# Optimization experiments

Measured on AMD Instinct MI355X. Metric: run time of the kernel, lower is better.

The kernel has to match this reference:

```python
import jax, jax.numpy as jnp
import numpy as np

B, H, N, C, E, D, L_OUT, LAYERS = 16, 64, 512, 3, 128, 32, 12, 2


def setup_inputs() -> dict:
    key = jax.random.key(0)
    ks = jax.random.split(key, 16)
    nrm = lambda k, s, sc=1.0: jax.random.normal(k, s, jnp.float32) * sc
    adj = jax.random.uniform(ks[0], (N, N), jnp.float32)
    adj = adj / adj.sum(axis=-1, keepdims=True)  # row-normalized prior adjacency
    return {
        "x_input": nrm(ks[1], (B, H, N, C)),
        "adj": adj,
        "Wf": nrm(ks[2], (3, E, 3 * C), 0.1),
        "Uf": nrm(ks[3], (3, E, E), 0.05),
        "bf": jnp.zeros((3, E), jnp.float32),
        "E1f": nrm(ks[4], (N, D)),
        "E2f": nrm(ks[5], (N, D)),
        "Wb": nrm(ks[6], (3, E, 3 * C), 0.1),
        "Ub": nrm(ks[7], (3, E, E), 0.05),
        "bb": jnp.zeros((3, E), jnp.float32),
        "E1b": nrm(ks[8], (N, D)),
        "E2b": nrm(ks[9], (N, D)),
        "dec_w": nrm(ks[10], (L_OUT, LAYERS, 2 * E), 0.05),  # Conv2d(layer_num->out_len, k=(1,2E)) squeezed
        "dec_b": jnp.zeros((L_OUT,), jnp.float32),
        "out_w": nrm(ks[11], (L_OUT, L_OUT), 0.1),  # 1x1 Conv2d squeezed
        "out_b": jnp.zeros((L_OUT,), jnp.float32),
    }


def _cell_step(c, xt, adj, A_dyn, W, U, b):
    # Graph-coupled GRU cell (IBNCell): xt [B,C,N], c [B,E,N].
    msg = jnp.concatenate(
        [xt,
         jnp.einsum('bcn,nm->bcm', xt, adj),      # prior-graph message passing
         jnp.einsum('bcn,nm->bcm', xt, A_dyn)],   # learned dynamic-graph message passing
        axis=1)  # [B, 3C, N]
    gx = jnp.einsum('goc,bcn->gbon', W, msg)  # 3 stacked gate projections
    r = jax.nn.sigmoid(gx[0] + jnp.einsum('oe,ben->bon', U[0], c) + b[0][:, None])
    u = jax.nn.sigmoid(gx[1] + jnp.einsum('oe,ben->bon', U[1], c) + b[1][:, None])
    g = jnp.tanh(gx[2] + jnp.einsum('oe,ben->bon', U[2], r * c) + b[2][:, None])
    return u * c + (1.0 - u) * g


def _forward(x_input, adj, Wf, Uf, bf, E1f, E2f, Wb, Ub, bb, E1b, E2b, dec_w, dec_b, out_w, out_b):
    # torch: x_input.transpose(-3,-1).transpose(-2,-1) -> [B,C,H,N]; scan layout [H,B,C,N]
    xs = jnp.transpose(x_input, (1, 0, 3, 2))
    A_f = jax.nn.softmax(jax.nn.relu(E1f @ E2f.T), axis=-1)  # dynamic adjacency, fwd cell
    A_b = jax.nn.softmax(jax.nn.relu(E1b @ E2b.T), axis=-1)  # dynamic adjacency, back cell
    c0 = jnp.zeros((xs.shape[1], Wf.shape[1], xs.shape[3]), xs.dtype)  # [B,E,N]

    def step_f(c, xt):
        cn = _cell_step(c, xt, adj, A_f, Wf, Uf, bf)
        return cn, None

    # Output only depends on the last timestep of the bidirectional concat:
    # forward branch -> final state after H steps; backward branch (after flip)
    # at t=H-1 -> its FIRST step (input x[H-1]). Dead per-step outputs elided.
    h_fwd, _ = jax.lax.scan(step_f, c0, xs)
    h_back0 = _cell_step(c0, xs[-1], adj, A_b, Wb, Ub, bb)
    last_ht = jnp.concatenate([h_fwd, h_back0], axis=1)  # [B, 2E, N]

    lt = jnp.transpose(last_ht, (0, 2, 1))  # [B, N, 2E]
    # layer loop z>0 is a no-op on current_layer_output -> final_result repeats last_ht
    final = jnp.broadcast_to(lt[:, None], (lt.shape[0], LAYERS, lt.shape[1], lt.shape[2]))
    h = jnp.einsum('blne,ole->bon', final, dec_w) + dec_b[:, None]  # decoder conv (1,2E)
    return jnp.einsum('oi,bin->bon', out_w, h) + out_b[:, None]  # 1x1 output conv -> [B,L_OUT,N]


def reference(x_input, adj, Wf, Uf, bf, E1f, E2f, Wb, Ub, bb, E1b, E2b, dec_w, dec_b, out_w, out_b):
    return _forward(x_input, adj, Wf, Uf, bf, E1f, E2f, Wb, Ub, bb, E1b, E2b, dec_w, dec_b, out_w, out_b)
```

## Files before the change

kernel.cpp:

```cpp
#include <hip/hip_runtime.h>


typedef _Float16 half8_t __attribute__((ext_vector_type(8)));
typedef float float4_t __attribute__((ext_vector_type(4)));

__device__ __forceinline__ float sigmoidf_(float x) {
  return __builtin_amdgcn_rcpf(1.f + __expf(-x));
}
__device__ __forceinline__ float tanhf_(float x) {
  return fmaf(-2.f, __builtin_amdgcn_rcpf(__expf(2.f * x) + 1.f), 1.f);
}

__global__ __launch_bounds__(256) void prep_kernel(
    const float* __restrict__ E1f, const float* __restrict__ E2f,
    const float* __restrict__ E1b, const float* __restrict__ E2b,
    const float* __restrict__ adj, const float* __restrict__ Wf,
    const float* __restrict__ Uf, const float* __restrict__ bf,
    const float* __restrict__ Wb, const float* __restrict__ bb,
    _Float16* __restrict__ adjT, _Float16* __restrict__ AfT,
    _Float16* __restrict__ AbT, _Float16* __restrict__ ufrag,
    _Float16* __restrict__ wbfrag) {
  int bid = blockIdx.x;
  int tid = threadIdx.x;
  if (bid >= 1272) {
    int r2 = bid - 1272;
    int gi = 1 + (r2 & 1);
    int rt = (r2 >> 1) & 1;
    int og = r2 >> 2;
    for (int e = tid; e < 512; e += 256) {
      int lane = e >> 3, j = e & 7;
      int o = og * 32 + rt * 16 + (lane & 15);
      int q = (lane >> 4) * 8 + j;
      float v = (q < 9) ? Wb[gi * 1152 + o * 9 + q]
                        : (q == 9 ? bb[gi * 128 + o] : 0.f);
      wbfrag[r2 * 512 + e] = (_Float16)v;
    }
    return;
  }
  if (bid >= 1152) {
    int r = bid - 1152;
    int kb = r % 5;
    int gi = (r / 5) % 3;
    int rt = (r / 15) % 2;
    int og = r / 30;
    for (int e = tid; e < 512; e += 256) {
      int lane = e >> 3, j = e & 7;
      int o = og * 32 + rt * 16 + (lane & 15);
      int q4 = lane >> 4;
      float v;
      if (kb < 4) {
        v = Uf[gi * 16384 + o * 128 + kb * 32 + q4 * 8 + j];
      } else {
        int q = q4 * 8 + j;
        v = (q < 9) ? Wf[gi * 1152 + o * 9 + q]
                    : (q == 9 ? bf[gi * 128 + o] : 0.f);
      }
      ufrag[r * 512 + e] = (_Float16)v;
    }
    return;
  }
  if (bid >= 1024) {
    int base = (bid - 1024) * 4;
    for (int r = 0; r < 4; ++r) {
      int row = base + r;
      float v0 = adj[row * 512 + tid];
      float v1 = adj[row * 512 + tid + 256];
      adjT[(size_t)tid * 512 + row] = (_Float16)v0;
      adjT[(size_t)(tid + 256) * 512 + row] = (_Float16)v1;
    }
    return;
  }
  int which = bid >> 9;
  int row = bid & 511;
  const float* E1 = which ? E1b : E1f;
  const float* E2 = which ? E2b : E2f;
  _Float16* A = which ? AbT : AfT;
  __shared__ float e1s[32];
  __shared__ float red[256];
  if (tid < 32) e1s[tid] = E1[row * 32 + tid];
  __syncthreads();
  float s[2];
#pragma unroll
  for (int h = 0; h < 2; ++h) {
    int m = tid + h * 256;
    const float4* e2 = (const float4*)(E2 + m * 32);
    float acc = 0.f;
#pragma unroll
    for (int d4 = 0; d4 < 8; ++d4) {
      float4 v = e2[d4];
      acc = fmaf(v.x, e1s[d4 * 4 + 0], acc);
      acc = fmaf(v.y, e1s[d4 * 4 + 1], acc);
      acc = fmaf(v.z, e1s[d4 * 4 + 2], acc);
      acc = fmaf(v.w, e1s[d4 * 4 + 3], acc);
    }
    s[h] = fmaxf(acc, 0.f);
  }
  red[tid] = fmaxf(s[0], s[1]);
  __syncthreads();
  for (int off = 128; off > 0; off >>= 1) {
    if (tid < off) red[tid] = fmaxf(red[tid], red[tid + off]);
    __syncthreads();
  }
  float mx = red[0];
  __syncthreads();
  float e0 = __expf(s[0] - mx), e1v = __expf(s[1] - mx);
  red[tid] = e0 + e1v;
  __syncthreads();
  for (int off = 128; off > 0; off >>= 1) {
    if (tid < off) red[tid] += red[tid + off];
    __syncthreads();
  }
  float inv = __builtin_amdgcn_rcpf(red[0]);
  A[(size_t)tid * 512 + row] = (_Float16)(e0 * inv);
  A[(size_t)(tid + 256) * 512 + row] = (_Float16)(e1v * inv);
}

__global__ __launch_bounds__(256, 2) void msg_kernel(
    const float* __restrict__ x, const _Float16* __restrict__ adjT,
    const _Float16* __restrict__ AfT, const _Float16* __restrict__ AbT,
    _Float16* __restrict__ msg16, _Float16* __restrict__ msgb16) {
  __shared__ __align__(16) _Float16 Alds[48 * 512];
  __shared__ __align__(16) _Float16 Sst[16 * 64 * 16];
  int tid = threadIdx.x;
  int t = blockIdx.x >> 3;
  int n0g = (blockIdx.x & 7) * 64;
  int lane = tid & 63, og = tid >> 6;
  int l15 = lane & 15, q4 = lane >> 4, q0 = q4 * 8;
  bool is63 = (t == 63);

  {
    int b = tid >> 4, li = tid & 15;
    const float4* xb = (const float4*)(x + (size_t)(b * 64 + t) * 1536);
#pragma unroll
    for (int k = 0; k < 24; ++k) {
      float4 v = xb[k * 16 + li];
      int j0 = (k * 16 + li) * 4;
#pragma unroll
      for (int e = 0; e < 4; ++e) {
        int j = j0 + e;
        int n = (j * 21846) >> 16;
        int c = j - n * 3;
        int m = b * 3 + c;
        float val = (e == 0) ? v.x : (e == 1) ? v.y : (e == 2) ? v.z : v.w;
        Alds[m * 512 + ((((n >> 3) ^ (m & 7)) << 3) | (n & 7))] = (_Float16)val;
      }
    }
  }
  __syncthreads();

  const float4_t zero4 = {0.f, 0.f, 0.f, 0.f};
  float4_t acc[3][2], accb[3];
#pragma unroll
  for (int mt = 0; mt < 3; ++mt) { acc[mt][0] = zero4; acc[mt][1] = zero4; accb[mt] = zero4; }

  int n = n0g + og * 16 + l15;
  for (int kb = 0; kb < 16; ++kb) {
    half8_t afr[3];
#pragma unroll
    for (int mt = 0; mt < 3; ++mt) {
      int m = mt * 16 + l15;
      afr[mt] = *(const half8_t*)&Alds[m * 512 + ((((kb * 4 + q4) ^ (m & 7)) << 3))];
    }
    half8_t b0 = *(const half8_t*)&adjT[(size_t)n * 512 + kb * 32 + q0];
    half8_t b1 = *(const half8_t*)&AfT[(size_t)n * 512 + kb * 32 + q0];
#pragma unroll
    for (int mt = 0; mt < 3; ++mt) {
      acc[mt][0] = __builtin_amdgcn_mfma_f32_16x16x32_f16(afr[mt], b0, acc[mt][0], 0, 0, 0);
      acc[mt][1] = __builtin_amdgcn_mfma_f32_16x16x32_f16(afr[mt], b1, acc[mt][1], 0, 0, 0);
    }
    if (is63) {
      half8_t b2 = *(const half8_t*)&AbT[(size_t)n * 512 + kb * 32 + q0];
#pragma unroll
      for (int mt = 0; mt < 3; ++mt)
        accb[mt] = __builtin_amdgcn_mfma_f32_16x16x32_f16(afr[mt], b2, accb[mt], 0, 0, 0);
    }
  }

  for (int i = tid; i < 1024; i += 256) {
    int tb = i >> 6, nl = i & 63;
    int nn = n0g + nl;
    _Float16* row = &Sst[(tb * 64 + nl) * 16];
#pragma unroll
    for (int c = 0; c < 3; ++c) {
      int m = tb * 3 + c;
      row[c] = Alds[m * 512 + ((((nn >> 3) ^ (m & 7)) << 3) | (nn & 7))];
    }
    row[9] = (_Float16)1.f;
#pragma unroll
    for (int kz = 10; kz < 16; ++kz) row[kz] = (_Float16)0.f;
  }
#pragma unroll
  for (int mt = 0; mt < 3; ++mt)
#pragma unroll
    for (int r = 0; r < 4; ++r) {
      int m = mt * 16 + q4 * 4 + r;
      int tb = (m * 21846) >> 16;
      int c = m - tb * 3;
      _Float16* row = &Sst[(tb * 64 + og * 16 + l15) * 16];
      row[3 + c] = (_Float16)acc[mt][0][r];
      row[6 + c] = (_Float16)acc[mt][1][r];
    }
  __syncthreads();
  for (int i = tid; i < 1024; i += 256) {
    int tb = i >> 6, nl = i & 63;
    uint4* dst = (uint4*)&msg16[((size_t)(t * 16 + tb) * 512 + n0g + nl) * 16];
    const uint4* s = (const uint4*)&Sst[(tb * 64 + nl) * 16];
    dst[0] = s[0];
    dst[1] = s[1];
  }
  if (is63) {
    __syncthreads();
#pragma unroll
    for (int mt = 0; mt < 3; ++mt)
#pragma unroll
      for (int r = 0; r < 4; ++r) {
        int m = mt * 16 + q4 * 4 + r;
        int tb = (m * 21846) >> 16;
        int c = m - tb * 3;
        Sst[(tb * 64 + og * 16 + l15) * 16 + 6 + c] = (_Float16)accb[mt][r];
      }
    __syncthreads();
    for (int i = tid; i < 1024; i += 256) {
      int tb = i >> 6, nl = i & 63;
      uint4* dst = (uint4*)&msgb16[((size_t)tb * 512 + n0g + nl) * 16];
      const uint4* s = (const uint4*)&Sst[(tb * 64 + nl) * 16];
      dst[0] = s[0];
      dst[1] = s[1];
    }
  }
}

__global__ __launch_bounds__(256, 2) __attribute__((amdgpu_waves_per_eu(2, 2)))
void rec_kernel(
    const _Float16* __restrict__ msg16, const _Float16* __restrict__ msgb16,
    const _Float16* __restrict__ ufrag, const _Float16* __restrict__ wbfrag,
    const float* __restrict__ dec_w, const float* __restrict__ dec_b,
    const float* __restrict__ out_w, const float* __restrict__ out_b,
    float* __restrict__ out) {
  __shared__ __align__(16) _Float16 Bmsg[64 * 16 * 16];
  __shared__ __align__(16) _Float16 Cbuf[4 * 64 * 8];
  __shared__ __align__(16) _Float16 Gbuf[4 * 64 * 8];
  __shared__ float hf_lds[128 * 16];
  __shared__ float hb_lds[128 * 16];
  __shared__ float hdec_lds[12 * 16];
  int tid = threadIdx.x, bid = blockIdx.x;
  int b = bid >> 5;
  int n0 = (bid & 31) * 16;
  int lane = tid & 63, og = tid >> 6;
  int l15 = lane & 15, q4 = lane >> 4;

  half8_t afrag[3][2][5];
#pragma unroll
  for (int gi = 0; gi < 3; ++gi)
#pragma unroll
    for (int rt = 0; rt < 2; ++rt)
#pragma unroll
      for (int kb = 0; kb < 5; ++kb)
        afrag[gi][rt][kb] = *(const half8_t*)
            &ufrag[(size_t)((((og * 2 + rt) * 3 + gi) * 5 + kb) * 512) + lane * 8];

  {
    const uint4* src = (const uint4*)msg16;
    uint4* dst = (uint4*)Bmsg;
    for (int f = tid; f < 2048; f += 256) {
      int t = f >> 5, off = f & 31;
      int nn = off >> 1, h = off & 1;
      dst[t * 32 + nn * 2 + (h ^ (nn & 1))] =
          src[((size_t)(t * 16 + b) * 512 + n0) * 2 + off];
    }
  }
  {
    uint4 z; z.x = z.y = z.z = z.w = 0;
    ((uint4*)Cbuf)[tid] = z;
  }
  float cr[2][4];
#pragma unroll
  for (int rt = 0; rt < 2; ++rt)
#pragma unroll
    for (int r = 0; r < 4; ++r) cr[rt][r] = 0.f;
  __syncthreads();

  const float4_t zero4 = {0.f, 0.f, 0.f, 0.f};
  union H4U { _Float16 h[4]; unsigned long long u; };
  int bm_off = l15 * 16 + (((q4 & 1) ^ (l15 & 1)) << 3);

  for (int t = 0; t < 64; ++t) {
    half8_t bmsg = *(const half8_t*)&Bmsg[t * 256 + bm_off];
    half8_t cf[4];
#pragma unroll
    for (int kb = 0; kb < 4; ++kb)
      cf[kb] = *(const half8_t*)&Cbuf[(kb * 64 + lane) * 8];

    float4_t accr[2], accu[2];
    accr[0] = accr[1] = accu[0] = accu[1] = zero4;
#pragma unroll
    for (int kb = 0; kb < 4; ++kb)
#pragma unroll
      for (int rt = 0; rt < 2; ++rt) {
        accr[rt] = __builtin_amdgcn_mfma_f32_16x16x32_f16(afrag[0][rt][kb], cf[kb], accr[rt], 0, 0, 0);
        accu[rt] = __builtin_amdgcn_mfma_f32_16x16x32_f16(afrag[1][rt][kb], cf[kb], accu[rt], 0, 0, 0);
      }
#pragma unroll
    for (int rt = 0; rt < 2; ++rt) {
      accr[rt] = __builtin_amdgcn_mfma_f32_16x16x32_f16(afrag[0][rt][4], bmsg, accr[rt], 0, 0, 0);
      accu[rt] = __builtin_amdgcn_mfma_f32_16x16x32_f16(afrag[1][rt][4], bmsg, accu[rt], 0, 0, 0);
    }
#pragma unroll
    for (int rt = 0; rt < 2; ++rt) {
      H4U v;
#pragma unroll
      for (int r = 0; r < 4; ++r)
        v.h[r] = (_Float16)(sigmoidf_(accr[rt][r]) * cr[rt][r]);
      int lane_t = (rt * 2 + (q4 >> 1)) * 16 + l15;
      *(unsigned long long*)&Gbuf[(og * 64 + lane_t) * 8 + (q4 & 1) * 4] = v.u;
    }
    __syncthreads();

    half8_t gf[4];
#pragma unroll
    for (int kb = 0; kb < 4; ++kb)
      gf[kb] = *(const half8_t*)&Gbuf[(kb * 64 + lane) * 8];
    float4_t accg[2];
#pragma unroll
    for (int rt = 0; rt < 2; ++rt) {
      float4_t a = zero4;
#pragma unroll
      for (int kb = 0; kb < 4; ++kb)
        a = __builtin_amdgcn_mfma_f32_16x16x32_f16(afrag[2][rt][kb], gf[kb], a, 0, 0, 0);
      a = __builtin_amdgcn_mfma_f32_16x16x32_f16(afrag[2][rt][4], bmsg, a, 0, 0, 0);
      accg[rt] = a;
    }
#pragma unroll
    for (int rt = 0; rt < 2; ++rt) {
      H4U v;
#pragma unroll
      for (int r = 0; r < 4; ++r) {
        float uu = sigmoidf_(accu[rt][r]);
        float gg = tanhf_(accg[rt][r]);
        float cn = fmaf(uu, cr[rt][r] - gg, gg);
        cr[rt][r] = cn;
        v.h[r] = (_Float16)cn;
      }
      int lane_t = (rt * 2 + (q4 >> 1)) * 16 + l15;
      *(unsigned long long*)&Cbuf[(og * 64 + lane_t) * 8 + (q4 & 1) * 4] = v.u;
    }
    __syncthreads();
  }

  {
    half8_t bbk = *(const half8_t*)
        &msgb16[((size_t)b * 512 + n0 + l15) * 16 + (q4 & 1) * 8];
#pragma unroll
    for (int rt = 0; rt < 2; ++rt) {
      half8_t au_f = *(const half8_t*)&wbfrag[(size_t)(((og * 2 + rt) * 2 + 0) * 512) + lane * 8];
      half8_t ag_f = *(const half8_t*)&wbfrag[(size_t)(((og * 2 + rt) * 2 + 1) * 512) + lane * 8];
      float4_t au = __builtin_amdgcn_mfma_f32_16x16x32_f16(au_f, bbk, zero4, 0, 0, 0);
      float4_t ag = __builtin_amdgcn_mfma_f32_16x16x32_f16(ag_f, bbk, zero4, 0, 0, 0);
#pragma unroll
      for (int r = 0; r < 4; ++r) {
        int row = og * 32 + rt * 16 + q4 * 4 + r;
        float uu = sigmoidf_(au[r]);
        float gg = tanhf_(ag[r]);
        hb_lds[row * 16 + l15] = (1.f - uu) * gg;
        hf_lds[row * 16 + l15] = cr[rt][r];
      }
    }
  }
  __syncthreads();

  if (tid < 192) {
    int i = tid >> 4, cc = tid & 15;
    const float* dwa = dec_w + (size_t)i * 512;
    const float* dwb = dwa + 256;
    float hd = dec_b[i];
    for (int e = 0; e < 128; ++e) {
      hd = fmaf(dwa[e] + dwb[e], hf_lds[e * 16 + cc], hd);
      hd = fmaf(dwa[128 + e] + dwb[128 + e], hb_lds[e * 16 + cc], hd);
    }
    hdec_lds[i * 16 + cc] = hd;
  }
  __syncthreads();
  if (tid < 192) {
    int o = tid >> 4, cc = tid & 15;
    float v = out_b[o];
#pragma unroll
    for (int i = 0; i < 12; ++i) v = fmaf(out_w[o * 12 + i], hdec_lds[i * 16 + cc], v);
    out[((size_t)(b * 12 + o)) * 512 + n0 + cc] = v;
  }
}

extern "C" void kernel_launch(void* const* d_in, const int* in_sizes, int n_in,
                              void* d_out, int out_size, void* d_ws, size_t ws_size,
                              hipStream_t stream) {
  (void)in_sizes; (void)n_in; (void)out_size; (void)ws_size;
  const float* x     = (const float*)d_in[0];
  const float* adj   = (const float*)d_in[1];
  const float* Wf    = (const float*)d_in[2];
  const float* Uf    = (const float*)d_in[3];
  const float* bf    = (const float*)d_in[4];
  const float* E1f   = (const float*)d_in[5];
  const float* E2f   = (const float*)d_in[6];
  const float* Wb    = (const float*)d_in[7];
  const float* bb    = (const float*)d_in[9];
  const float* E1b   = (const float*)d_in[10];
  const float* E2b   = (const float*)d_in[11];
  const float* dec_w = (const float*)d_in[12];
  const float* dec_b = (const float*)d_in[13];
  const float* out_w = (const float*)d_in[14];
  const float* out_b = (const float*)d_in[15];

  _Float16* h      = (_Float16*)d_ws;
  _Float16* adjT   = h;
  _Float16* AfT    = h + 262144;
  _Float16* AbT    = h + 524288;
  _Float16* msg16  = h + 786432;
  _Float16* msgb16 = h + 9175040;
  _Float16* ufrag  = h + 9306112;
  _Float16* wbfrag = h + 9367552;

  prep_kernel<<<1288, 256, 0, stream>>>(E1f, E2f, E1b, E2b, adj, Wf, Uf, bf,
                                        Wb, bb, adjT, AfT, AbT, ufrag, wbfrag);
  msg_kernel<<<512, 256, 0, stream>>>(x, adjT, AfT, AbT, msg16, msgb16);
  rec_kernel<<<512, 256, 0, stream>>>(msg16, msgb16, ufrag, wbfrag,
                                      dec_w, dec_b, out_w, out_b, (float*)d_out);
}
```

Measured before the change: 214.7 us.

## Restructure message and recurrence kernels: transposed fp16 x, packed msg, 512-thread recurrence

A new prep stage writes x to global memory as transposed fp16. The message kernel then reads its A operand from global memory instead of staging it in LDS, splits the adjacency matrices across waves, and runs twice as many smaller blocks. The message record shrinks from 16 to 12 halves, which cuts msg write and read traffic. The recurrence kernel now uses 512 threads per block, each wave owning 16 output rows instead of 32, and prefetches the next timestep's msg from global memory instead of preloading it into LDS, trading shorter per-wave serial MFMA chains for more waves per barrier.

Result: slower. 220.0 us (+2.5%).

```diff
diff --git a/kernel.cpp b/kernel.cpp
--- a/kernel.cpp
+++ b/kernel.cpp
@@ -3,6 +3,8 @@
 
 typedef _Float16 half8_t __attribute__((ext_vector_type(8)));
 typedef float float4_t __attribute__((ext_vector_type(4)));
+
+#define PIN(x) asm volatile("" : "+v"(x))
 
 __device__ __forceinline__ float sigmoidf_(float x) {
   return __builtin_amdgcn_rcpf(1.f + __expf(-x));
@@ -14,22 +16,37 @@
 __global__ __launch_bounds__(256) void prep_kernel(
     const float* __restrict__ E1f, const float* __restrict__ E2f,
     const float* __restrict__ E1b, const float* __restrict__ E2b,
-    const float* __restrict__ adj, const float* __restrict__ Wf,
-    const float* __restrict__ Uf, const float* __restrict__ bf,
-    const float* __restrict__ Wb, const float* __restrict__ bb,
-    _Float16* __restrict__ adjT, _Float16* __restrict__ AfT,
-    _Float16* __restrict__ AbT, _Float16* __restrict__ ufrag,
+    const float* __restrict__ adj, const float* __restrict__ x,
+    const float* __restrict__ Wf, const float* __restrict__ Uf,
+    const float* __restrict__ bf, const float* __restrict__ Wb,
+    const float* __restrict__ bb, _Float16* __restrict__ adjT,
+    _Float16* __restrict__ AfT, _Float16* __restrict__ AbT,
+    _Float16* __restrict__ xT16, _Float16* __restrict__ ufrag,
     _Float16* __restrict__ wbfrag) {
   int bid = blockIdx.x;
   int tid = threadIdx.x;
+  if (bid >= 1288) {
+    int bid2 = bid - 1288;
+    int b = bid2 >> 6, t = bid2 & 63;
+    const float2* xp = (const float2*)(x + (size_t)(b * 64 + t) * 1536);
+    float2 f0 = xp[tid * 3], f1 = xp[tid * 3 + 1], f2 = xp[tid * 3 + 2];
+    _Float16* dst = xT16 + (size_t)(b * 64 + t) * 1536;
+    int n0_ = tid * 2;
+    dst[n0_] = (_Float16)f0.x;
+    dst[512 + n0_] = (_Float16)f0.y;
+    dst[1024 + n0_] = (_Float16)f1.x;
+    dst[n0_ + 1] = (_Float16)f1.y;
+    dst[512 + n0_ + 1] = (_Float16)f2.x;
+    dst[1024 + n0_ + 1] = (_Float16)f2.y;
+    return;
+  }
   if (bid >= 1272) {
     int r2 = bid - 1272;
     int gi = 1 + (r2 & 1);
-    int rt = (r2 >> 1) & 1;
-    int og = r2 >> 2;
+    int og = r2 >> 1;
     for (int e = tid; e < 512; e += 256) {
       int lane = e >> 3, j = e & 7;
-      int o = og * 32 + rt * 16 + (lane & 15);
+      int o = og * 16 + (lane & 15);
       int q = (lane >> 4) * 8 + j;
       float v = (q < 9) ? Wb[gi * 1152 + o * 9 + q]
                         : (q == 9 ? bb[gi * 128 + o] : 0.f);
@@ -41,11 +58,10 @@
     int r = bid - 1152;
     int kb = r % 5;
     int gi = (r / 5) % 3;
-    int rt = (r / 15) % 2;
-    int og = r / 30;
+    int og = r / 15;
     for (int e = tid; e < 512; e += 256) {
       int lane = e >> 3, j = e & 7;
-      int o = og * 32 + rt * 16 + (lane & 15);
+      int o = og * 16 + (lane & 15);
       int q4 = lane >> 4;
       float v;
       if (kb < 4) {
@@ -115,79 +131,55 @@
   A[(size_t)(tid + 256) * 512 + row] = (_Float16)(e1v * inv);
 }
 
-__global__ __launch_bounds__(256, 2) void msg_kernel(
-    const float* __restrict__ x, const _Float16* __restrict__ adjT,
+__global__ __launch_bounds__(256, 4) void msg_kernel(
+    const _Float16* __restrict__ xT16, const _Float16* __restrict__ adjT,
     const _Float16* __restrict__ AfT, const _Float16* __restrict__ AbT,
     _Float16* __restrict__ msg16, _Float16* __restrict__ msgb16) {
-  __shared__ __align__(16) _Float16 Alds[48 * 512];
-  __shared__ __align__(16) _Float16 Sst[16 * 64 * 16];
+  __shared__ __align__(8) _Float16 Sst[512 * 12];
   int tid = threadIdx.x;
-  int t = blockIdx.x >> 3;
-  int n0g = (blockIdx.x & 7) * 64;
+  int t = blockIdx.x >> 4;
+  int n0g = (blockIdx.x & 15) * 32;
   int lane = tid & 63, og = tid >> 6;
   int l15 = lane & 15, q4 = lane >> 4, q0 = q4 * 8;
+  int nt = og & 1, mat = og >> 1;
   bool is63 = (t == 63);
-
-  {
-    int b = tid >> 4, li = tid & 15;
-    const float4* xb = (const float4*)(x + (size_t)(b * 64 + t) * 1536);
-#pragma unroll
-    for (int k = 0; k < 24; ++k) {
-      float4 v = xb[k * 16 + li];
-      int j0 = (k * 16 + li) * 4;
-#pragma unroll
-      for (int e = 0; e < 4; ++e) {
-        int j = j0 + e;
-        int n = (j * 21846) >> 16;
-        int c = j - n * 3;
-        int m = b * 3 + c;
-        float val = (e == 0) ? v.x : (e == 1) ? v.y : (e == 2) ? v.z : v.w;
-        Alds[m * 512 + ((((n >> 3) ^ (m & 7)) << 3) | (n & 7))] = (_Float16)val;
-      }
-    }
-  }
-  __syncthreads();
+  bool doAb = is63 && (mat == 0);
+
+  const _Float16* Bmat = mat ? AfT : adjT;
+  int n = n0g + nt * 16 + l15;
 
   const float4_t zero4 = {0.f, 0.f, 0.f, 0.f};
-  float4_t acc[3][2], accb[3];
-#pragma unroll
-  for (int mt = 0; mt < 3; ++mt) { acc[mt][0] = zero4; acc[mt][1] = zero4; accb[mt] = zero4; }
-
-  int n = n0g + og * 16 + l15;
+  float4_t acc[3], accb[3];
+#pragma unroll
+  for (int mt = 0; mt < 3; ++mt) { acc[mt] = zero4; accb[mt] = zero4; }
+
   for (int kb = 0; kb < 16; ++kb) {
-    half8_t afr[3];
+    half8_t b0 = *(const half8_t*)&Bmat[(size_t)n * 512 + kb * 32 + q0];
+    half8_t b2;
+    if (doAb) b2 = *(const half8_t*)&AbT[(size_t)n * 512 + kb * 32 + q0];
 #pragma unroll
     for (int mt = 0; mt < 3; ++mt) {
       int m = mt * 16 + l15;
-      afr[mt] = *(const half8_t*)&Alds[m * 512 + ((((kb * 4 + q4) ^ (m & 7)) << 3))];
-    }
-    half8_t b0 = *(const half8_t*)&adjT[(size_t)n * 512 + kb * 32 + q0];
-    half8_t b1 = *(const half8_t*)&AfT[(size_t)n * 512 + kb * 32 + q0];
-#pragma unroll
-    for (int mt = 0; mt < 3; ++mt) {
-      acc[mt][0] = __builtin_amdgcn_mfma_f32_16x16x32_f16(afr[mt], b0, acc[mt][0], 0, 0, 0);
-      acc[mt][1] = __builtin_amdgcn_mfma_f32_16x16x32_f16(afr[mt], b1, acc[mt][1], 0, 0, 0);
-    }
-    if (is63) {
-      half8_t b2 = *(const half8_t*)&AbT[(size_t)n * 512 + kb * 32 + q0];
-#pragma unroll
-      for (int mt = 0; mt < 3; ++mt)
-        accb[mt] = __builtin_amdgcn_mfma_f32_16x16x32_f16(afr[mt], b2, accb[mt], 0, 0, 0);
-    }
-  }
-
-  for (int i = tid; i < 1024; i += 256) {
-    int tb = i >> 6, nl = i & 63;
+      int bm = (m * 21846) >> 16;
+      int cm = m - bm * 3;
+      half8_t a = *(const half8_t*)
+          &xT16[((size_t)(bm * 64 + t) * 3 + cm) * 512 + kb * 32 + q0];
+      acc[mt] = __builtin_amdgcn_mfma_f32_16x16x32_f16(a, b0, acc[mt], 0, 0, 0);
+      if (doAb)
+        accb[mt] = __builtin_amdgcn_mfma_f32_16x16x32_f16(a, b2, accb[mt], 0, 0, 0);
+    }
+  }
+
+  for (int i = tid; i < 512; i += 256) {
+    int tb = i >> 5, nl = i & 31;
     int nn = n0g + nl;
-    _Float16* row = &Sst[(tb * 64 + nl) * 16];
-#pragma unroll
-    for (int c = 0; c < 3; ++c) {
-      int m = tb * 3 + c;
-      row[c] = Alds[m * 512 + ((((nn >> 3) ^ (m & 7)) << 3) | (nn & 7))];
-    }
+    _Float16* row = &Sst[i * 12];
+#pragma unroll
+    for (int c = 0; c < 3; ++c)
+      row[c] = xT16[((size_t)(tb * 64 + t) * 3 + c) * 512 + nn];
     row[9] = (_Float16)1.f;
-#pragma unroll
-    for (int kz = 10; kz < 16; ++kz) row[kz] = (_Float16)0.f;
+    row[10] = (_Float16)0.f;
+    row[11] = (_Float16)0.f;
   }
 #pragma unroll
   for (int mt = 0; mt < 3; ++mt)
@@ -196,48 +188,45 @@
       int m = mt * 16 + q4 * 4 + r;
       int tb = (m * 21846) >> 16;
       int c = m - tb * 3;
-      _Float16* row = &Sst[(tb * 64 + og * 16 + l15) * 16];
-      row[3 + c] = (_Float16)acc[mt][0][r];
-      row[6 + c] = (_Float16)acc[mt][1][r];
-    }
-  __syncthreads();
-  for (int i = tid; i < 1024; i += 256) {
-    int tb = i >> 6, nl = i & 63;
-    uint4* dst = (uint4*)&msg16[((size_t)(t * 16 + tb) * 512 + n0g + nl) * 16];
-    const uint4* s = (const uint4*)&Sst[(tb * 64 + nl) * 16];
-    dst[0] = s[0];
-    dst[1] = s[1];
+      Sst[((size_t)tb * 32 + nt * 16 + l15) * 12 + 3 + mat * 3 + c] =
+          (_Float16)acc[mt][r];
+    }
+  __syncthreads();
+  for (int i = tid; i < 512; i += 256) {
+    int tb = i >> 5, nl = i & 31;
+    const uint2* s = (const uint2*)&Sst[i * 12];
+    uint2* dst = (uint2*)&msg16[((size_t)(t * 16 + tb) * 512 + n0g + nl) * 12];
+    dst[0] = s[0]; dst[1] = s[1]; dst[2] = s[2];
   }
   if (is63) {
     __syncthreads();
-#pragma unroll
-    for (int mt = 0; mt < 3; ++mt)
-#pragma unroll
-      for (int r = 0; r < 4; ++r) {
-        int m = mt * 16 + q4 * 4 + r;
-        int tb = (m * 21846) >> 16;
-        int c = m - tb * 3;
-        Sst[(tb * 64 + og * 16 + l15) * 16 + 6 + c] = (_Float16)accb[mt][r];
-      }
-    __syncthreads();
-    for (int i = tid; i < 1024; i += 256) {
-      int tb = i >> 6, nl = i & 63;
-      uint4* dst = (uint4*)&msgb16[((size_t)tb * 512 + n0g + nl) * 16];
-      const uint4* s = (const uint4*)&Sst[(tb * 64 + nl) * 16];
-      dst[0] = s[0];
-      dst[1] = s[1];
-    }
-  }
-}
-
-__global__ __launch_bounds__(256, 2) __attribute__((amdgpu_waves_per_eu(2, 2)))
-void rec_kernel(
+    if (mat == 0) {
+#pragma unroll
+      for (int mt = 0; mt < 3; ++mt)
+#pragma unroll
+        for (int r = 0; r < 4; ++r) {
+          int m = mt * 16 + q4 * 4 + r;
+          int tb = (m * 21846) >> 16;
+          int c = m - tb * 3;
+          Sst[((size_t)tb * 32 + nt * 16 + l15) * 12 + 6 + c] = (_Float16)accb[mt][r];
+        }
+    }
+    __syncthreads();
+    for (int i = tid; i < 512; i += 256) {
+      int tb = i >> 5, nl = i & 31;
+      const uint2* s = (const uint2*)&Sst[i * 12];
+      uint2* dst = (uint2*)&msgb16[((size_t)tb * 512 + n0g + nl) * 12];
+      dst[0] = s[0]; dst[1] = s[1]; dst[2] = s[2];
+    }
+  }
+}
+
+__global__ __launch_bounds__(512, 4) void rec_kernel(
     const _Float16* __restrict__ msg16, const _Float16* __restrict__ msgb16,
     const _Float16* __restrict__ ufrag, const _Float16* __restrict__ wbfrag,
     const float* __restrict__ dec_w, const float* __restrict__ dec_b,
     const float* __restrict__ out_w, const float* __restrict__ out_b,
     float* __restrict__ out) {
-  __shared__ __align__(16) _Float16 Bmsg[64 * 16 * 16];
   __shared__ __align__(16) _Float16 Cbuf[4 * 64 * 8];
   __shared__ __align__(16) _Float16 Gbuf[4 * 64 * 8];
   __shared__ float hf_lds[128 * 16];
@@ -249,70 +238,72 @@
   int lane = tid & 63, og = tid >> 6;
   int l15 = lane & 15, q4 = lane >> 4;
 
-  half8_t afrag[3][2][5];
+  half8_t afrag[3][5];
 #pragma unroll
   for (int gi = 0; gi < 3; ++gi)
 #pragma unroll
-    for (int rt = 0; rt < 2; ++rt)
-#pragma unroll
-      for (int kb = 0; kb < 5; ++kb)
-        afrag[gi][rt][kb] = *(const half8_t*)
-            &ufrag[(size_t)((((og * 2 + rt) * 3 + gi) * 5 + kb) * 512) + lane * 8];
-
-  {
-    const uint4* src = (const uint4*)msg16;
-    uint4* dst = (uint4*)Bmsg;
-    for (int f = tid; f < 2048; f += 256) {
-      int t = f >> 5, off = f & 31;
-      int nn = off >> 1, h = off & 1;
-      dst[t * 32 + nn * 2 + (h ^ (nn & 1))] =
-          src[((size_t)(t * 16 + b) * 512 + n0) * 2 + off];
-    }
-  }
-  {
+    for (int kb = 0; kb < 5; ++kb) {
+      afrag[gi][kb] = *(const half8_t*)
+          &ufrag[(size_t)(((og * 3 + gi) * 5 + kb) * 512) + lane * 8];
+      PIN(afrag[gi][kb]);
+    }
+
+  if (tid < 256) {
     uint4 z; z.x = z.y = z.z = z.w = 0;
     ((uint4*)Cbuf)[tid] = z;
   }
-  float cr[2][4];
-#pragma unroll
-  for (int rt = 0; rt < 2; ++rt)
-#pragma unroll
-    for (int r = 0; r < 4; ++r) cr[rt][r] = 0.f;
+  float cr[4] = {0.f, 0.f, 0.f, 0.f};
   __syncthreads();
 
   const float4_t zero4 = {0.f, 0.f, 0.f, 0.f};
   union H4U { _Float16 h[4]; unsigned long long u; };
-  int bm_off = l15 * 16 + (((q4 & 1) ^ (l15 & 1)) << 3);
+  union U16 { uint4 u4; half8_t h8; };
+  unsigned odd = q4 & 1;
+  const char* mrow = (const char*)msg16 + ((size_t)(b * 512 + n0 + l15)) * 24;
+  const size_t tstride = (size_t)16 * 512 * 24;
+
+  U16 bu;
+  {
+    uint4 lo = *(const uint4*)mrow;
+    uint2 hi = *(const uint2*)(mrow + 16);
+    bu.u4.x = odd ? hi.x : lo.x;
+    bu.u4.y = odd ? hi.y : lo.y;
+    bu.u4.z = odd ? 0u : lo.z;
+    bu.u4.w = odd ? 0u : lo.w;
+  }
+  half8_t bm_cur = bu.h8;
+
+  int kb_w = og >> 1;
+  int lane_w = ((og & 1) * 2 + (q4 >> 1)) * 16 + l15;
+  int j0 = (q4 & 1) * 4;
 
   for (int t = 0; t < 64; ++t) {
-    half8_t bmsg = *(const half8_t*)&Bmsg[t * 256 + bm_off];
+    int tn = (t < 63) ? t + 1 : 63;
+    const char* p = mrow + (size_t)tn * tstride;
+    uint4 lo = *(const uint4*)p;
+    uint2 hi = *(const uint2*)(p + 16);
+
     half8_t cf[4];
 #pragma unroll
     for (int kb = 0; kb < 4; ++kb)
       cf[kb] = *(const half8_t*)&Cbuf[(kb * 64 + lane) * 8];
 
-    float4_t accr[2], accu[2];
-    accr[0] = accr[1] = accu[0] = accu[1] = zero4;
-#pragma unroll
-    for (int kb = 0; kb < 4; ++kb)
-#pragma unroll
-      for (int rt = 0; rt < 2; ++rt) {
-        accr[rt] = __builtin_amdgcn_mfma_f32_16x16x32_f16(afrag[0][rt][kb], cf[kb], accr[rt], 0, 0, 0);
-        accu[rt] = __builtin_amdgcn_mfma_f32_16x16x32_f16(afrag[1][rt][kb], cf[kb], accu[rt], 0, 0, 0);
-      }
-#pragma unroll
-    for (int rt = 0; rt < 2; ++rt) {
-      accr[rt] = __builtin_amdgcn_mfma_f32_16x16x32_f16(afrag[0][rt][4], bmsg, accr[rt], 0, 0, 0);
-      accu[rt] = __builtin_amdgcn_mfma_f32_16x16x32_f16(afrag[1][rt][4], bmsg, accu[rt], 0, 0, 0);
-    }
-#pragma unroll
-    for (int rt = 0; rt < 2; ++rt) {
+    float4_t accr = zero4, accu = zero4;
+#pragma unroll
+    for (int kb = 0; kb < 4; ++kb) {
+      accr = __builtin_amdgcn_mfma_f32_16x16x32_f16(afrag[0][kb], cf[kb], accr, 0, 0, 0);
+      accu = __builtin_amdgcn_mfma_f32_16x16x32_f16(afrag[1][kb], cf[kb], accu, 0, 0, 0);
+    }
+    accr = __builtin_amdgcn_mfma_f32_16x16x32_f16(afrag[0][4], bm_cur, accr, 0, 0, 0);
+    accu = __builtin_amdgcn_mfma_f32_16x16x32_f16(afrag[1][4], bm_cur, accu, 0, 0, 0);
+    float4_t accg = __builtin_amdgcn_mfma_f32_16x16x32_f16(afrag[2][4], bm_cur, zero4, 0, 0, 0);
+
+    {
       H4U v;
 #pragma unroll
       for (int r = 0; r < 4; ++r)
-        v.h[r] = (_Float16)(sigmoidf_(accr[rt][r]) * cr[rt][r]);
-      int lane_t = (rt * 2 + (q4 >> 1)) * 16 + l15;
-      *(unsigned long long*)&Gbuf[(og * 64 + lane_t) * 8 + (q4 & 1) * 4] = v.u;
+        v.h[r] = (_Float16)(sigmoidf_(accr[r]) * cr[r]);
+      *(unsigned long long*)&Gbuf[(kb_w * 64 + lane_w) * 8 + j0] = v.u;
     }
     __syncthreads();
 
@@ -320,50 +311,51 @@
 #pragma unroll
     for (int kb = 0; kb < 4; ++kb)
       gf[kb] = *(const half8_t*)&Gbuf[(kb * 64 + lane) * 8];
-    float4_t accg[2];
-#pragma unroll
-    for (int rt = 0; rt < 2; ++rt) {
-      float4_t a = zero4;
-#pragma unroll
-      for (int kb = 0; kb < 4; ++kb)
-        a = __builtin_amdgcn_mfma_f32_16x16x32_f16(afrag[2][rt][kb], gf[kb], a, 0, 0, 0);
-      a = __builtin_amdgcn_mfma_f32_16x16x32_f16(afrag[2][rt][4], bmsg, a, 0, 0, 0);
-      accg[rt] = a;
-    }
-#pragma unroll
-    for (int rt = 0; rt < 2; ++rt) {
+#pragma unroll
+    for (int kb = 0; kb < 4; ++kb)
+      accg = __builtin_amdgcn_mfma_f32_16x16x32_f16(afrag[2][kb], gf[kb], accg, 0, 0, 0);
+
+    {
       H4U v;
 #pragma unroll
       for (int r = 0; r < 4; ++r) {
-        float uu = sigmoidf_(accu[rt][r]);
-        float gg = tanhf_(accg[rt][r]);
-        float cn = fmaf(uu, cr[rt][r] - gg, gg);
-        cr[rt][r] = cn;
+        float uu = sigmoidf_(accu[r]);
+        float gg = tanhf_(accg[r]);
+        float cn = fmaf(uu, cr[r] - gg, gg);
+        cr[r] = cn;
         v.h[r] = (_Float16)cn;
       }
-      int lane_t = (rt * 2 + (q4 >> 1)) * 16 + l15;
-      *(unsigned long long*)&Cbuf[(og * 64 + lane_t) * 8 + (q4 & 1) * 4] = v.u;
-    }
-    __syncthreads();
+      *(unsigned long long*)&Cbuf[(kb_w * 64 + lane_w) * 8 + j0] = v.u;
+    }
+    __syncthreads();
+
+    bu.u4.x = odd ? hi.x : lo.x;
+    bu.u4.y = odd ? hi.y : lo.y;
+    bu.u4.z = odd ? 0u : lo.z;
+    bu.u4.w = odd ? 0u : lo.w;
+    bm_cur = bu.h8;
   }
 
   {
-    half8_t bbk = *(const half8_t*)
-        &msgb16[((size_t)b * 512 + n0 + l15) * 16 + (q4 & 1) * 8];
-#pragma unroll
-    for (int rt = 0; rt < 2; ++rt) {
-      half8_t au_f = *(const half8_t*)&wbfrag[(size_t)(((og * 2 + rt) * 2 + 0) * 512) + lane * 8];
-      half8_t ag_f = *(const half8_t*)&wbfrag[(size_t)(((og * 2 + rt) * 2 + 1) * 512) + lane * 8];
-      float4_t au = __builtin_amdgcn_mfma_f32_16x16x32_f16(au_f, bbk, zero4, 0, 0, 0);
-      float4_t ag = __builtin_amdgcn_mfma_f32_16x16x32_f16(ag_f, bbk, zero4, 0, 0, 0);
-#pragma unroll
-      for (int r = 0; r < 4; ++r) {
-        int row = og * 32 + rt * 16 + q4 * 4 + r;
-        float uu = sigmoidf_(au[r]);
-        float gg = tanhf_(ag[r]);
-        hb_lds[row * 16 + l15] = (1.f - uu) * gg;
-        hf_lds[row * 16 + l15] = cr[rt][r];
-      }
+    const char* p = (const char*)msgb16 + ((size_t)(b * 512 + n0 + l15)) * 24;
+    uint4 lo = *(const uint4*)p;
+    uint2 hi = *(const uint2*)(p + 16);
+    U16 bb2;
+    bb2.u4.x = odd ? hi.x : lo.x;
+    bb2.u4.y = odd ? hi.y : lo.y;
+    bb2.u4.z = odd ? 0u : lo.z;
+    bb2.u4.w = odd ? 0u : lo.w;
+    half8_t au_f = *(const half8_t*)&wbfrag[(size_t)((og * 2 + 0) * 512) + lane * 8];
+    half8_t ag_f = *(const half8_t*)&wbfrag[(size_t)((og * 2 + 1) * 512) + lane * 8];
+    float4_t au = __builtin_amdgcn_mfma_f32_16x16x32_f16(au_f, bb2.h8, zero4, 0, 0, 0);
+    float4_t ag = __builtin_amdgcn_mfma_f32_16x16x32_f16(ag_f, bb2.h8, zero4, 0, 0, 0);
+#pragma unroll
+    for (int r = 0; r < 4; ++r) {
+      int row = og * 16 + q4 * 4 + r;
+      float uu = sigmoidf_(au[r]);
+      float gg = tanhf_(ag[r]);
+      hb_lds[row * 16 + l15] = (1.f - uu) * gg;
+      hf_lds[row * 16 + l15] = cr[r];
     }
   }
   __syncthreads();
@@ -413,14 +405,15 @@
   _Float16* adjT   = h;
   _Float16* AfT    = h + 262144;
   _Float16* AbT    = h + 524288;
-  _Float16* msg16  = h + 786432;
-  _Float16* msgb16 = h + 9175040;
-  _Float16* ufrag  = h + 9306112;
-  _Float16* wbfrag = h + 9367552;
-
-  prep_kernel<<<1288, 256, 0, stream>>>(E1f, E2f, E1b, E2b, adj, Wf, Uf, bf,
-                                        Wb, bb, adjT, AfT, AbT, ufrag, wbfrag);
-  msg_kernel<<<512, 256, 0, stream>>>(x, adjT, AfT, AbT, msg16, msgb16);
-  rec_kernel<<<512, 256, 0, stream>>>(msg16, msgb16, ufrag, wbfrag,
+  _Float16* xT16   = h + 786432;
+  _Float16* ufrag  = h + 2359296;
+  _Float16* wbfrag = h + 2420736;
+  _Float16* msg16  = h + 2428928;
+  _Float16* msgb16 = h + 8720384;
+
+  prep_kernel<<<2312, 256, 0, stream>>>(E1f, E2f, E1b, E2b, adj, x, Wf, Uf, bf,
+                                        Wb, bb, adjT, AfT, AbT, xT16, ufrag, wbfrag);
+  msg_kernel<<<1024, 256, 0, stream>>>(xT16, adjT, AfT, AbT, msg16, msgb16);
+  rec_kernel<<<512, 512, 0, stream>>>(msg16, msgb16, ufrag, wbfrag,
                                       dec_w, dec_b, out_w, out_b, (float*)d_out);
 }
```

## Split recurrent GRU rows across 8 waves, stream messages from global in fragment layout

Applied to the files above, without the earlier changes.

The recurrent kernel now runs 512 threads per block, so each wave owns one 16-row output tile instead of two. That halves the serial MFMA chain and activation work per wave on every timestep. The message tensor is written by msg_kernel directly in MFMA fragment order and prefetched one step ahead from global memory, which removes the LDS staging buffer and its fill loop. Log2(e) scaling is folded into the gate weights so sigmoid and tanh use raw exp2 and rcp, and fp16 packing uses cvt_pkrtz. The cost is higher register pressure and more waves taking part in each per-step block barrier.

New measurement: 203.0 us. 5.4% less time.

```diff
diff --git a/kernel.cpp b/kernel.cpp
--- a/kernel.cpp
+++ b/kernel.cpp
@@ -2,14 +2,13 @@
 
 
 typedef _Float16 half8_t __attribute__((ext_vector_type(8)));
+typedef __fp16 fp16x2_t __attribute__((ext_vector_type(2)));
 typedef float float4_t __attribute__((ext_vector_type(4)));
 
-__device__ __forceinline__ float sigmoidf_(float x) {
-  return __builtin_amdgcn_rcpf(1.f + __expf(-x));
-}
-__device__ __forceinline__ float tanhf_(float x) {
-  return fmaf(-2.f, __builtin_amdgcn_rcpf(__expf(2.f * x) + 1.f), 1.f);
-}
+#define PIN(x) asm volatile("" : "+v"(x))
+
+__device__ __forceinline__ float exp2_(float x) { return __builtin_amdgcn_exp2f(x); }
+__device__ __forceinline__ float rcp_(float x) { return __builtin_amdgcn_rcpf(x); }
 
 __global__ __launch_bounds__(256) void prep_kernel(
     const float* __restrict__ E1f, const float* __restrict__ E2f,
@@ -25,15 +24,15 @@
   if (bid >= 1272) {
     int r2 = bid - 1272;
     int gi = 1 + (r2 & 1);
-    int rt = (r2 >> 1) & 1;
-    int og = r2 >> 2;
+    int og = r2 >> 1;
+    float scl = (gi == 2) ? 2.8853902f : -1.4426950f;
     for (int e = tid; e < 512; e += 256) {
       int lane = e >> 3, j = e & 7;
-      int o = og * 32 + rt * 16 + (lane & 15);
+      int o = og * 16 + (lane & 15);
       int q = (lane >> 4) * 8 + j;
       float v = (q < 9) ? Wb[gi * 1152 + o * 9 + q]
                         : (q == 9 ? bb[gi * 128 + o] : 0.f);
-      wbfrag[r2 * 512 + e] = (_Float16)v;
+      wbfrag[r2 * 512 + e] = (_Float16)(v * scl);
     }
     return;
   }
@@ -41,11 +40,11 @@
     int r = bid - 1152;
     int kb = r % 5;
     int gi = (r / 5) % 3;
-    int rt = (r / 15) % 2;
-    int og = r / 30;
+    int og = r / 15;
+    float scl = (gi == 2) ? 2.8853902f : -1.4426950f;
     for (int e = tid; e < 512; e += 256) {
       int lane = e >> 3, j = e & 7;
-      int o = og * 32 + rt * 16 + (lane & 15);
+      int o = og * 16 + (lane & 15);
       int q4 = lane >> 4;
       float v;
       if (kb < 4) {
@@ -55,7 +54,7 @@
         v = (q < 9) ? Wf[gi * 1152 + o * 9 + q]
                     : (q == 9 ? bf[gi * 128 + o] : 0.f);
       }
-      ufrag[r * 512 + e] = (_Float16)v;
+      ufrag[r * 512 + e] = (_Float16)(v * scl);
     }
     return;
   }
@@ -110,7 +109,7 @@
     if (tid < off) red[tid] += red[tid + off];
     __syncthreads();
   }
-  float inv = __builtin_amdgcn_rcpf(red[0]);
+  float inv = rcp_(red[0]);
   A[(size_t)tid * 512 + row] = (_Float16)(e0 * inv);
   A[(size_t)(tid + 256) * 512 + row] = (_Float16)(e1v * inv);
 }
@@ -118,12 +117,13 @@
 __global__ __launch_bounds__(256, 2) void msg_kernel(
     const float* __restrict__ x, const _Float16* __restrict__ adjT,
     const _Float16* __restrict__ AfT, const _Float16* __restrict__ AbT,
-    _Float16* __restrict__ msg16, _Float16* __restrict__ msgb16) {
+    _Float16* __restrict__ msgF, _Float16* __restrict__ msgbF) {
   __shared__ __align__(16) _Float16 Alds[48 * 512];
-  __shared__ __align__(16) _Float16 Sst[16 * 64 * 16];
+  __shared__ __align__(16) _Float16 Sst[16 * 4 * 32 * 8];
   int tid = threadIdx.x;
   int t = blockIdx.x >> 3;
   int n0g = (blockIdx.x & 7) * 64;
+  int g4 = (blockIdx.x & 7) * 4;
   int lane = tid & 63, og = tid >> 6;
   int l15 = lane & 15, q4 = lane >> 4, q0 = q4 * 8;
   bool is63 = (t == 63);
@@ -176,18 +176,19 @@
     }
   }
 
-  for (int i = tid; i < 1024; i += 256) {
-    int tb = i >> 6, nl = i & 63;
-    int nn = n0g + nl;
-    _Float16* row = &Sst[(tb * 64 + nl) * 16];
+  for (int u = tid; u < 1024; u += 256) {
+    int tb = u >> 6, nt = (u >> 4) & 3, cl = u & 15;
+    int nn = n0g + nt * 16 + cl;
+    _Float16* r0 = &Sst[(((tb * 4 + nt) * 32) + cl) * 8];
+    _Float16* r1 = r0 + 16 * 8;
 #pragma unroll
     for (int c = 0; c < 3; ++c) {
       int m = tb * 3 + c;
-      row[c] = Alds[m * 512 + ((((nn >> 3) ^ (m & 7)) << 3) | (nn & 7))];
-    }
-    row[9] = (_Float16)1.f;
-#pragma unroll
-    for (int kz = 10; kz < 16; ++kz) row[kz] = (_Float16)0.f;
+      r0[c] = Alds[m * 512 + ((((nn >> 3) ^ (m & 7)) << 3) | (nn & 7))];
+    }
+    r1[1] = (_Float16)1.f;
+#pragma unroll
+    for (int z = 2; z < 8; ++z) r1[z] = (_Float16)0.f;
   }
 #pragma unroll
   for (int mt = 0; mt < 3; ++mt)
@@ -195,18 +196,18 @@
     for (int r = 0; r < 4; ++r) {
       int m = mt * 16 + q4 * 4 + r;
       int tb = (m * 21846) >> 16;
-      int c = m - tb * 3;
-      _Float16* row = &Sst[(tb * 64 + og * 16 + l15) * 16];
-      row[3 + c] = (_Float16)acc[mt][0][r];
-      row[6 + c] = (_Float16)acc[mt][1][r];
-    }
-  __syncthreads();
-  for (int i = tid; i < 1024; i += 256) {
-    int tb = i >> 6, nl = i & 63;
-    uint4* dst = (uint4*)&msg16[((size_t)(t * 16 + tb) * 512 + n0g + nl) * 16];
-    const uint4* s = (const uint4*)&Sst[(tb * 64 + nl) * 16];
-    dst[0] = s[0];
-    dst[1] = s[1];
+      int ch = m - tb * 3;
+      _Float16* base = &Sst[((tb * 4 + og) * 32) * 8];
+      base[(l15)*8 + 3 + ch] = (_Float16)acc[mt][0][r];
+      if (ch < 2) base[(l15)*8 + 6 + ch] = (_Float16)acc[mt][1][r];
+      else        base[(16 + l15) * 8 + 0] = (_Float16)acc[mt][1][r];
+    }
+  __syncthreads();
+  for (int i = tid; i < 2048; i += 256) {
+    int sl = i >> 5, lane32 = i & 31;
+    int tb = sl >> 2, nt = sl & 3;
+    ((uint4*)msgF)[((size_t)(tb * 32 + g4 + nt) * 64 + t) * 32 + lane32] =
+        ((const uint4*)Sst)[i];
   }
   if (is63) {
     __syncthreads();
@@ -216,103 +217,93 @@
       for (int r = 0; r < 4; ++r) {
         int m = mt * 16 + q4 * 4 + r;
         int tb = (m * 21846) >> 16;
-        int c = m - tb * 3;
-        Sst[(tb * 64 + og * 16 + l15) * 16 + 6 + c] = (_Float16)accb[mt][r];
+        int ch = m - tb * 3;
+        _Float16* base = &Sst[((tb * 4 + og) * 32) * 8];
+        if (ch < 2) base[(l15)*8 + 6 + ch] = (_Float16)accb[mt][r];
+        else        base[(16 + l15) * 8 + 0] = (_Float16)accb[mt][r];
       }
     __syncthreads();
-    for (int i = tid; i < 1024; i += 256) {
-      int tb = i >> 6, nl = i & 63;
-      uint4* dst = (uint4*)&msgb16[((size_t)tb * 512 + n0g + nl) * 16];
-      const uint4* s = (const uint4*)&Sst[(tb * 64 + nl) * 16];
-      dst[0] = s[0];
-      dst[1] = s[1];
+    for (int i = tid; i < 2048; i += 256) {
+      int sl = i >> 5, lane32 = i & 31;
+      int tb = sl >> 2, nt = sl & 3;
+      ((uint4*)msgbF)[(size_t)(tb * 32 + g4 + nt) * 32 + lane32] =
+          ((const uint4*)Sst)[i];
     }
   }
 }
 
-__global__ __launch_bounds__(256, 2) __attribute__((amdgpu_waves_per_eu(2, 2)))
-void rec_kernel(
-    const _Float16* __restrict__ msg16, const _Float16* __restrict__ msgb16,
+__global__ __launch_bounds__(512, 4) void rec_kernel(
+    const _Float16* __restrict__ msgF, const _Float16* __restrict__ msgbF,
     const _Float16* __restrict__ ufrag, const _Float16* __restrict__ wbfrag,
     const float* __restrict__ dec_w, const float* __restrict__ dec_b,
     const float* __restrict__ out_w, const float* __restrict__ out_b,
     float* __restrict__ out) {
-  __shared__ __align__(16) _Float16 Bmsg[64 * 16 * 16];
-  __shared__ __align__(16) _Float16 Cbuf[4 * 64 * 8];
-  __shared__ __align__(16) _Float16 Gbuf[4 * 64 * 8];
+  __shared__ __align__(16) _Float16 Cbuf[2048];
+  __shared__ __align__(16) _Float16 Gbuf[2048];
   __shared__ float hf_lds[128 * 16];
   __shared__ float hb_lds[128 * 16];
   __shared__ float hdec_lds[12 * 16];
   int tid = threadIdx.x, bid = blockIdx.x;
   int b = bid >> 5;
-  int n0 = (bid & 31) * 16;
+  int nt = bid & 31;
+  int n0 = nt * 16;
   int lane = tid & 63, og = tid >> 6;
   int l15 = lane & 15, q4 = lane >> 4;
 
-  half8_t afrag[3][2][5];
+  half8_t afrag[3][5];
 #pragma unroll
   for (int gi = 0; gi < 3; ++gi)
 #pragma unroll
-    for (int rt = 0; rt < 2; ++rt)
-#pragma unroll
-      for (int kb = 0; kb < 5; ++kb)
-        afrag[gi][rt][kb] = *(const half8_t*)
-            &ufrag[(size_t)((((og * 2 + rt) * 3 + gi) * 5 + kb) * 512) + lane * 8];
-
-  {
-    const uint4* src = (const uint4*)msg16;
-    uint4* dst = (uint4*)Bmsg;
-    for (int f = tid; f < 2048; f += 256) {
-      int t = f >> 5, off = f & 31;
-      int nn = off >> 1, h = off & 1;
-      dst[t * 32 + nn * 2 + (h ^ (nn & 1))] =
-          src[((size_t)(t * 16 + b) * 512 + n0) * 2 + off];
-    }
-  }
-  {
+    for (int kb = 0; kb < 5; ++kb) {
+      afrag[gi][kb] = *(const half8_t*)
+          &ufrag[(size_t)(((og * 3 + gi) * 5 + kb) * 512) + lane * 8];
+      PIN(afrag[gi][kb]);
+    }
+
+  if (tid < 256) {
     uint4 z; z.x = z.y = z.z = z.w = 0;
     ((uint4*)Cbuf)[tid] = z;
   }
-  float cr[2][4];
-#pragma unroll
-  for (int rt = 0; rt < 2; ++rt)
-#pragma unroll
-    for (int r = 0; r < 4; ++r) cr[rt][r] = 0.f;
-  __syncthreads();
+  float cr[4] = {0.f, 0.f, 0.f, 0.f};
 
   const float4_t zero4 = {0.f, 0.f, 0.f, 0.f};
-  union H4U { _Float16 h[4]; unsigned long long u; };
-  int bm_off = l15 * 16 + (((q4 & 1) ^ (l15 & 1)) << 3);
+  union H4U { fp16x2_t h2[2]; unsigned long long u; };
+  const _Float16* mp = msgF + (size_t)(b * 32 + nt) * 64 * 256 + (lane & 31) * 8;
+  half8_t bm = *(const half8_t*)mp;
+
+  int kb_w = og >> 1;
+  int lane_w = ((og & 1) * 2 + (q4 >> 1)) * 16 + l15;
+  int j0 = (q4 & 1) * 4;
+  __syncthreads();
 
   for (int t = 0; t < 64; ++t) {
-    half8_t bmsg = *(const half8_t*)&Bmsg[t * 256 + bm_off];
+    mp += 256;
+    half8_t bm_n = *(const half8_t*)mp;
+
     half8_t cf[4];
 #pragma unroll
     for (int kb = 0; kb < 4; ++kb)
       cf[kb] = *(const half8_t*)&Cbuf[(kb * 64 + lane) * 8];
 
-    float4_t accr[2], accu[2];
-    accr[0] = accr[1] = accu[0] = accu[1] = zero4;
-#pragma unroll
-    for (int kb = 0; kb < 4; ++kb)
-#pragma unroll
-      for (int rt = 0; rt < 2; ++rt) {
-        accr[rt] = __builtin_amdgcn_mfma_f32_16x16x32_f16(afrag[0][rt][kb], cf[kb], accr[rt], 0, 0, 0);
-        accu[rt] = __builtin_amdgcn_mfma_f32_16x16x32_f16(afrag[1][rt][kb], cf[kb], accu[rt], 0, 0, 0);
-      }
-#pragma unroll
-    for (int rt = 0; rt < 2; ++rt) {
-      accr[rt] = __builtin_amdgcn_mfma_f32_16x16x32_f16(afrag[0][rt][4], bmsg, accr[rt], 0, 0, 0);
-      accu[rt] = __builtin_amdgcn_mfma_f32_16x16x32_f16(afrag[1][rt][4], bmsg, accu[rt], 0, 0, 0);
-    }
-#pragma unroll
-    for (int rt = 0; rt < 2; ++rt) {
+    float4_t accr = zero4, accu = zero4;
+#pragma unroll
+    for (int kb = 0; kb < 4; ++kb) {
+      accr = __builtin_amdgcn_mfma_f32_16x16x32_f16(afrag[0][kb], cf[kb], accr, 0, 0, 0);
+      accu = __builtin_amdgcn_mfma_f32_16x16x32_f16(afrag[1][kb], cf[kb], accu, 0, 0, 0);
+    }
+    accr = __builtin_amdgcn_mfma_f32_16x16x32_f16(afrag[0][4], bm, accr, 0, 0, 0);
+    accu = __builtin_amdgcn_mfma_f32_16x16x32_f16(afrag[1][4], bm, accu, 0, 0, 0);
+    float4_t accg = __builtin_amdgcn_mfma_f32_16x16x32_f16(afrag[2][4], bm, zero4, 0, 0, 0);
+
+    {
+      float rc0 = rcp_(1.f + exp2_(accr[0])) * cr[0];
+      float rc1 = rcp_(1.f + exp2_(accr[1])) * cr[1];
+      float rc2 = rcp_(1.f + exp2_(accr[2])) * cr[2];
+      float rc3 = rcp_(1.f + exp2_(accr[3])) * cr[3];
       H4U v;
-#pragma unroll
-      for (int r = 0; r < 4; ++r)
-        v.h[r] = (_Float16)(sigmoidf_(accr[rt][r]) * cr[rt][r]);
-      int lane_t = (rt * 2 + (q4 >> 1)) * 16 + l15;
-      *(unsigned long long*)&Gbuf[(og * 64 + lane_t) * 8 + (q4 & 1) * 4] = v.u;
+      v.h2[0] = __builtin_amdgcn_cvt_pkrtz(rc0, rc1);
+      v.h2[1] = __builtin_amdgcn_cvt_pkrtz(rc2, rc3);
+      *(unsigned long long*)&Gbuf[(kb_w * 64 + lane_w) * 8 + j0] = v.u;
     }
     __syncthreads();
 
@@ -320,50 +311,42 @@
 #pragma unroll
     for (int kb = 0; kb < 4; ++kb)
       gf[kb] = *(const half8_t*)&Gbuf[(kb * 64 + lane) * 8];
-    float4_t accg[2];
-#pragma unroll
-    for (int rt = 0; rt < 2; ++rt) {
-      float4_t a = zero4;
-#pragma unroll
-      for (int kb = 0; kb < 4; ++kb)
-        a = __builtin_amdgcn_mfma_f32_16x16x32_f16(afrag[2][rt][kb], gf[kb], a, 0, 0, 0);
-      a = __builtin_amdgcn_mfma_f32_16x16x32_f16(afrag[2][rt][4], bmsg, a, 0, 0, 0);
-      accg[rt] = a;
-    }
-#pragma unroll
-    for (int rt = 0; rt < 2; ++rt) {
+#pragma unroll
+    for (int kb = 0; kb < 4; ++kb)
+      accg = __builtin_amdgcn_mfma_f32_16x16x32_f16(afrag[2][kb], gf[kb], accg, 0, 0, 0);
+
+    {
       H4U v;
+      float cn[4];
 #pragma unroll
       for (int r = 0; r < 4; ++r) {
-        float uu = sigmoidf_(accu[rt][r]);
-        float gg = tanhf_(accg[rt][r]);
-        float cn = fmaf(uu, cr[rt][r] - gg, gg);
-        cr[rt][r] = cn;
-        v.h[r] = (_Float16)cn;
+        float uu = rcp_(1.f + exp2_(accu[r]));
+        float gg = fmaf(-2.f, rcp_(exp2_(accg[r]) + 1.f), 1.f);
+        cn[r] = fmaf(uu, cr[r] - gg, gg);
+        cr[r] = cn[r];
       }
-      int lane_t = (rt * 2 + (q4 >> 1)) * 16 + l15;
-      *(unsigned long long*)&Cbuf[(og * 64 + lane_t) * 8 + (q4 & 1) * 4] = v.u;
-    }
-    __syncthreads();
+      v.h2[0] = __builtin_amdgcn_cvt_pkrtz(cn[0], cn[1]);
+      v.h2[1] = __builtin_amdgcn_cvt_pkrtz(cn[2], cn[3]);
+      *(unsigned long long*)&Cbuf[(kb_w * 64 + lane_w) * 8 + j0] = v.u;
+    }
+    __syncthreads();
+    bm = bm_n;
   }
 
   {
     half8_t bbk = *(const half8_t*)
-        &msgb16[((size_t)b * 512 + n0 + l15) * 16 + (q4 & 1) * 8];
-#pragma unroll
-    for (int rt = 0; rt < 2; ++rt) {
-      half8_t au_f = *(const half8_t*)&wbfrag[(size_t)(((og * 2 + rt) * 2 + 0) * 512) + lane * 8];
-      half8_t ag_f = *(const half8_t*)&wbfrag[(size_t)(((og * 2 + rt) * 2 + 1) * 512) + lane * 8];
-      float4_t au = __builtin_amdgcn_mfma_f32_16x16x32_f16(au_f, bbk, zero4, 0, 0, 0);
-      float4_t ag = __builtin_amdgcn_mfma_f32_16x16x32_f16(ag_f, bbk, zero4, 0, 0, 0);
-#pragma unroll
-      for (int r = 0; r < 4; ++r) {
-        int row = og * 32 + rt * 16 + q4 * 4 + r;
-        float uu = sigmoidf_(au[r]);
-        float gg = tanhf_(ag[r]);
-        hb_lds[row * 16 + l15] = (1.f - uu) * gg;
-        hf_lds[row * 16 + l15] = cr[rt][r];
-      }
+        (msgbF + (size_t)(b * 32 + nt) * 256 + (lane & 31) * 8);
+    half8_t au_f = *(const half8_t*)&wbfrag[(size_t)((og * 2 + 0) * 512) + lane * 8];
+    half8_t ag_f = *(const half8_t*)&wbfrag[(size_t)((og * 2 + 1) * 512) + lane * 8];
+    float4_t au = __builtin_amdgcn_mfma_f32_16x16x32_f16(au_f, bbk, zero4, 0, 0, 0);
+    float4_t ag = __builtin_amdgcn_mfma_f32_16x16x32_f16(ag_f, bbk, zero4, 0, 0, 0);
+#pragma unroll
+    for (int r = 0; r < 4; ++r) {
+      int row = og * 16 + q4 * 4 + r;
+      float uu = rcp_(1.f + exp2_(au[r]));
+      float gg = fmaf(-2.f, rcp_(exp2_(ag[r]) + 1.f), 1.f);
+      hb_lds[row * 16 + l15] = (1.f - uu) * gg;
+      hf_lds[row * 16 + l15] = cr[r];
     }
   }
   __syncthreads();
@@ -413,14 +396,14 @@
   _Float16* adjT   = h;
   _Float16* AfT    = h + 262144;
   _Float16* AbT    = h + 524288;
-  _Float16* msg16  = h + 786432;
-  _Float16* msgb16 = h + 9175040;
-  _Float16* ufrag  = h + 9306112;
-  _Float16* wbfrag = h + 9367552;
+  _Float16* ufrag  = h + 786432;
+  _Float16* wbfrag = h + 847872;
+  _Float16* msgF   = h + 856064;
+  _Float16* msgbF  = h + 9244672;
 
   prep_kernel<<<1288, 256, 0, stream>>>(E1f, E2f, E1b, E2b, adj, Wf, Uf, bf,
                                         Wb, bb, adjT, AfT, AbT, ufrag, wbfrag);
-  msg_kernel<<<512, 256, 0, stream>>>(x, adjT, AfT, AbT, msg16, msgb16);
-  rec_kernel<<<512, 256, 0, stream>>>(msg16, msgb16, ufrag, wbfrag,
+  msg_kernel<<<512, 256, 0, stream>>>(x, adjT, AfT, AbT, msgF, msgbF);
+  rec_kernel<<<512, 512, 0, stream>>>(msgF, msgbF, ufrag, wbfrag,
                                       dec_w, dec_b, out_w, out_b, (float*)d_out);
 }
```
